# Kernel tuning notes

Measured on AMD Instinct MI355X. Metric: run time of the kernel, lower is better.

Reference implementation:

```python
import jax, jax.numpy as jnp
import numpy as np

N_EMBD = 2048
HEAD_DIM = 128
N_CTX = 2048
BATCH = 8
SEQ = 2048


def setup_inputs() -> dict:
    key = jax.random.key(0)
    ks = jax.random.split(key, 7)
    s = 1.0 / np.sqrt(N_EMBD)
    x = jax.random.normal(ks[0], (BATCH, SEQ, N_EMBD), dtype=jnp.float32)
    # torch Linear params: weight (out, in), bias (out,)
    Wq = jax.random.uniform(ks[1], (HEAD_DIM, N_EMBD), jnp.float32, -s, s)
    bq = jax.random.uniform(ks[2], (HEAD_DIM,), jnp.float32, -s, s)
    Wk = jax.random.uniform(ks[3], (HEAD_DIM, N_EMBD), jnp.float32, -s, s)
    bk = jax.random.uniform(ks[4], (HEAD_DIM,), jnp.float32, -s, s)
    Wv = jax.random.uniform(ks[5], (HEAD_DIM, N_EMBD), jnp.float32, -s, s)
    bv = jax.random.uniform(ks[6], (HEAD_DIM,), jnp.float32, -s, s)
    return {"x": x, "Wq": Wq, "bq": bq, "Wk": Wk, "bk": bk, "Wv": Wv, "bv": bv}


def reference(x, Wq, bq, Wk, bk, Wv, bv):
    # projections: y = x @ W^T + b
    q = jnp.einsum('bse,de->bsd', x, Wq) + bq  # (B, S, D)
    k = jnp.einsum('bse,de->bsd', x, Wk) + bk
    v = jnp.einsum('bse,de->bsd', x, Wv) + bv
    seq = x.shape[1]
    scores = jnp.einsum('bqd,bkd->bqk', q, k)  # (B, S, S)
    # causal mask: strictly-upper-triangular positions set to -inf (before scaling, as in source)
    causal = jnp.triu(jnp.ones((seq, seq), dtype=bool), k=1)
    scores = jnp.where(causal[None, :, :], -jnp.inf, scores)
    # NOTE: source scales by sqrt(seq_size), not sqrt(head_dim)
    weight = jax.nn.softmax(scores / jnp.sqrt(jnp.float32(seq)), axis=-1)
    return jnp.einsum('bqk,bkd->bqd', weight, v)
```

## Files before the change

kernel.cpp:

```cpp
#include <hip/hip_runtime.h>
#include <cmath>

#define BATCH 8
#define SEQ   2048
#define NEMB  2048
#define HD    128
#define NROWS (BATCH * SEQ)

typedef __bf16 v8bf __attribute__((ext_vector_type(8)));
typedef float  f32x4 __attribute__((ext_vector_type(4)));

union U8 { v8bf v; __bf16 b[8]; unsigned short e[8]; };
union F4 { f32x4 v; float f[4]; };

__device__ inline void async16(void* lds, const void* g) {
  __builtin_amdgcn_global_load_lds(
      (const __attribute__((address_space(1))) unsigned int*)g,
      (__attribute__((address_space(3))) unsigned int*)lds, 16, 0, 0);
}

__device__ inline v8bf cvt8(float4 a, float4 b) {
  U8 u;
  u.b[0] = (__bf16)a.x; u.b[1] = (__bf16)a.y; u.b[2] = (__bf16)a.z; u.b[3] = (__bf16)a.w;
  u.b[4] = (__bf16)b.x; u.b[5] = (__bf16)b.y; u.b[6] = (__bf16)b.z; u.b[7] = (__bf16)b.w;
  return u.v;
}

__global__ __launch_bounds__(256) void wconv_kernel(
    const float* __restrict__ Wq, const float* __restrict__ Wk,
    const float* __restrict__ Wv, __bf16* __restrict__ out) {
  const int id = blockIdx.x;
  const int proj = id >> 6, blk = id & 63;
  const float* __restrict__ W = proj == 0 ? Wq : proj == 1 ? Wk : Wv;
  __bf16* __restrict__ o = out + (size_t)proj * (HD * NEMB);
  const int base = blk * 4096 + threadIdx.x * 16;
  const float4* s = (const float4*)(W + base);
  float4 f0 = s[0], f1 = s[1], f2 = s[2], f3 = s[3];
  *(v8bf*)(o + base) = cvt8(f0, f1);
  *(v8bf*)(o + base + 8) = cvt8(f2, f3);
}

__global__ __launch_bounds__(512) void qkv_fused_kernel(
    const float* __restrict__ x, const __bf16* __restrict__ Wb,
    const float* __restrict__ bq, const float* __restrict__ bk,
    const float* __restrict__ bv,
    __bf16* __restrict__ Qb, __bf16* __restrict__ Kb, __bf16* __restrict__ Vb)
{
  const int bid0 = blockIdx.x;
  const int mt = ((bid0 & 7) << 5) + (bid0 >> 3);
  const int m0 = mt * 64;

  __shared__ char smem[131072];
  char* const A0 = smem;
  char* const A1 = smem + 16384;
  char* const Bu0 = smem + 32768;
  char* const Bu1 = smem + 81920;

  const int t = threadIdx.x, lane = t & 63, w = t >> 6;
  const int wm = w >> 2, wn4 = w & 3;
  const int hi = lane >> 4, lo = lane & 15;

  const float* pa[2];
  int laOff[2];
#pragma unroll
  for (int i = 0; i < 2; ++i) {
    const int j = w * 2 + i;
    const int r = j * 4 + (lane >> 4);
    const int c = (lane & 15) ^ (r & 7);
    pa[i] = x + (size_t)(m0 + r) * NEMB + c * 4;
    laOff[i] = j * 1024;
  }
  const __bf16* pb[6];
  int lbOff[6];
#pragma unroll
  for (int i = 0; i < 6; ++i) {
    const int j = w * 6 + i;
    const int r = j * 8 + (lane >> 3);
    const int pj = r >> 7, wr = r & 127;
    const int c = (lane & 7) ^ (r & 7);
    pb[i] = Wb + (size_t)pj * (HD * NEMB) + (size_t)wr * NEMB + c * 8;
    lbOff[i] = j * 1024;
  }

  f32x4 acc[2][6];
  const f32x4 fz = {0.f, 0.f, 0.f, 0.f};
#pragma unroll
  for (int m = 0; m < 2; ++m)
#pragma unroll
    for (int n = 0; n < 6; ++n) acc[m][n] = fz;

  auto STAGE = [&](int tt, char* Ab, char* Bb) {
    const int k0 = tt * 64;
#pragma unroll
    for (int i = 0; i < 2; ++i) async16(Ab + laOff[i], pa[i] + k0);
#pragma unroll
    for (int i = 0; i < 6; ++i) async16(Bb + lbOff[i], pb[i] + k0);
  };
  auto COMPUTE = [&](const char* Ab, const char* Bb) {
#pragma unroll
    for (int kk = 0; kk < 2; ++kk) {
      v8bf a[2], b[6];
#pragma unroll
      for (int m = 0; m < 2; ++m) {
        const int r = wm * 32 + m * 16 + lo;
        const int s = kk * 8 + hi * 2;
        const char* rowp = Ab + r * 256;
        F4 a0, a1;
        a0.v = *(const f32x4*)(rowp + (((s)     ^ (r & 7)) << 4));
        a1.v = *(const f32x4*)(rowp + (((s + 1) ^ (r & 7)) << 4));
        U8 u;
#pragma unroll
        for (int q = 0; q < 4; ++q) {
          u.b[q]     = (__bf16)a0.f[q];
          u.b[q + 4] = (__bf16)a1.f[q];
        }
        a[m] = u.v;
      }
      const int kc = kk * 4 + hi;
#pragma unroll
      for (int n = 0; n < 6; ++n) {
        const int r = wn4 * 96 + n * 16 + lo;
        b[n] = *(const v8bf*)(Bb + r * 128 + ((kc ^ (r & 7)) << 4));
      }
#pragma unroll
      for (int m = 0; m < 2; ++m)
#pragma unroll
        for (int n = 0; n < 6; ++n)
          acc[m][n] = __builtin_amdgcn_mfma_f32_16x16x32_bf16(a[m], b[n], acc[m][n], 0, 0, 0);
    }
  };

  const int NT = NEMB / 64;
  STAGE(0, A0, Bu0);
  for (int tt = 0; tt < NT; tt += 2) {
    __builtin_amdgcn_s_barrier();
    STAGE(tt + 1, A1, Bu1);
    asm volatile("s_waitcnt vmcnt(8)" ::: "memory");
    __builtin_amdgcn_s_barrier();
    COMPUTE(A0, Bu0);
    __builtin_amdgcn_s_barrier();
    if (tt + 2 < NT) {
      STAGE(tt + 2, A0, Bu0);
      asm volatile("s_waitcnt vmcnt(8)" ::: "memory");
    } else {
      asm volatile("s_waitcnt vmcnt(0)" ::: "memory");
    }
    __builtin_amdgcn_s_barrier();
    COMPUTE(A1, Bu1);
  }

#pragma unroll
  for (int n = 0; n < 6; ++n) {
    const int rrb = wn4 * 96 + n * 16;
    const int pj = rrb >> 7;
    const int col = (rrb & 127) + lo;
    __bf16* __restrict__ Out = pj == 0 ? Qb : pj == 1 ? Kb : Vb;
    const float* __restrict__ bias = pj == 0 ? bq : pj == 1 ? bk : bv;
    const float bi = bias[col];
#pragma unroll
    for (int m = 0; m < 2; ++m) {
#pragma unroll
      for (int r = 0; r < 4; ++r) {
        const int row = m0 + wm * 32 + m * 16 + hi * 4 + r;
        Out[(size_t)row * HD + col] = (__bf16)(acc[m][n][r] + bi);
      }
    }
  }
}

__global__ __launch_bounds__(256) void attn_kernel(
    const __bf16* __restrict__ Qb, const __bf16* __restrict__ Kb,
    const __bf16* __restrict__ Vb, __bf16* __restrict__ Opart,
    float* __restrict__ Ml)
{
  const int bid0 = blockIdx.x;
  const int bid = ((bid0 & 7) << 7) + (bid0 >> 3);
  const int b = bid >> 7;
  const int q = bid & 127;
  const int qt = q >> 2;
  const int s  = q & 3;
  const int q0 = qt * 64;
  const int kv_beg = (s * (qt + 1)) >> 2;
  const int kv_end = ((s + 1) * (qt + 1)) >> 2;
  const int nst = kv_end - kv_beg;

  const int t = threadIdx.x, lane = t & 63, w = t >> 6;
  const int hi = lane >> 4, lo = lane & 15;

  __shared__ __bf16 Ksm[2][64 * 128];
  __shared__ __bf16 Vtsm[2][128 * 64];
  __shared__ __bf16 Psm[4][16 * 64];

  v8bf aQ[4];
  {
    const __bf16* qp = Qb + ((size_t)(b * SEQ + q0 + w * 16 + lo)) * HD + hi * 8;
#pragma unroll
    for (int kk = 0; kk < 4; ++kk) aQ[kk] = *(const v8bf*)(qp + kk * 32);
  }

  const __bf16* kga[4];
#pragma unroll
  for (int i = 0; i < 4; ++i) {
    const int r = (w * 4 + i) * 4 + (lane >> 4);
    const int c = (lane & 15) ^ (r & 7);
    kga[i] = Kb + ((size_t)(b * SEQ) + r) * HD + c * 8;
  }

  const int keyg = t >> 4, dg = t & 15;
  U8 vv[4];

  f32x4 accO[8];
  const f32x4 fz = {0.f, 0.f, 0.f, 0.f};
#pragma unroll
  for (int n = 0; n < 8; ++n) accO[n] = fz;
  float m_s[4], l_s[4];
#pragma unroll
  for (int r = 0; r < 4; ++r) { m_s[r] = -INFINITY; l_s[r] = 0.f; }

  const float scale = 0.022097086912079608f;

  if (nst > 0) {
    auto STAGE_K = [&](int kv, int buf) {
      const size_t off = (size_t)kv * 64 * HD;
      char* kb = (char*)&Ksm[buf][0];
#pragma unroll
      for (int i = 0; i < 4; ++i) async16(kb + (w * 4 + i) * 1024, kga[i] + off);
    };
    auto LOAD_V = [&](int kv) {
      const __bf16* vp = Vb + ((size_t)(b * SEQ + kv * 64 + keyg * 4)) * HD + dg * 8;
#pragma unroll
      for (int j = 0; j < 4; ++j) vv[j].v = *(const v8bf*)(vp + (size_t)j * HD);
    };
    auto WRITE_VT = [&](int buf) {
      char* vb2 = (char*)&Vtsm[buf][0];
#pragma unroll
      for (int dd = 0; dd < 8; ++dd) {
        const int d = (dd + dg) & 7;
        ushort4 pk = make_ushort4(vv[0].e[d], vv[1].e[d], vv[2].e[d], vv[3].e[d]);
        const int row = dg * 8 + d;
        *(ushort4*)(vb2 + row * 128 + ((keyg * 8) ^ ((row & 7) << 4))) = pk;
      }
    };

    STAGE_K(kv_beg, 0);
    LOAD_V(kv_beg);
    WRITE_VT(0);
    __syncthreads();

    for (int t2 = 0; t2 < nst; ++t2) {
      const int kv = kv_beg + t2;
      const int cur = t2 & 1;
      const bool more = (t2 + 1 < nst);
      if (more) { STAGE_K(kv + 1, cur ^ 1); LOAD_V(kv + 1); }

      f32x4 accS[4];
#pragma unroll
      for (int n = 0; n < 4; ++n) accS[n] = fz;
      const char* ksm = (const char*)&Ksm[cur][0];
#pragma unroll
      for (int kk = 0; kk < 4; ++kk) {
        const int cb = kk * 64 + hi * 16;
        v8bf bk[4];
#pragma unroll
        for (int n = 0; n < 4; ++n) {
          const int r = n * 16 + lo;
          bk[n] = *(const v8bf*)(ksm + r * 256 + (cb ^ ((r & 7) << 4)));
        }
#pragma unroll
        for (int n = 0; n < 4; ++n)
          accS[n] = __builtin_amdgcn_mfma_f32_16x16x32_bf16(aQ[kk], bk[n], accS[n], 0, 0, 0);
      }

      float sv[4][4];
      const bool diag = (kv == qt);
#pragma unroll
      for (int n = 0; n < 4; ++n)
#pragma unroll
        for (int r = 0; r < 4; ++r) {
          float v = accS[n][r] * scale;
          if (diag) {
            const int key = kv * 64 + n * 16 + lo;
            const int qr = q0 + w * 16 + hi * 4 + r;
            if (key > qr) v = -INFINITY;
          }
          sv[n][r] = v;
        }

      float mx[4];
#pragma unroll
      for (int r = 0; r < 4; ++r) {
        mx[r] = fmaxf(fmaxf(sv[0][r], sv[1][r]), fmaxf(sv[2][r], sv[3][r]));
#pragma unroll
        for (int off = 1; off < 16; off <<= 1)
          mx[r] = fmaxf(mx[r], __shfl_xor(mx[r], off));
      }
      float corr[4], p[4][4], rs[4];
#pragma unroll
      for (int r = 0; r < 4; ++r) {
        const float mnew = fmaxf(m_s[r], mx[r]);
        corr[r] = __expf(m_s[r] - mnew);
        m_s[r] = mnew;
        rs[r] = 0.f;
      }
#pragma unroll
      for (int n = 0; n < 4; ++n)
#pragma unroll
        for (int r = 0; r < 4; ++r) {
          p[n][r] = __expf(sv[n][r] - m_s[r]);
          rs[r] += p[n][r];
        }
#pragma unroll
      for (int r = 0; r < 4; ++r) {
#pragma unroll
        for (int off = 1; off < 16; off <<= 1) rs[r] += __shfl_xor(rs[r], off);
        l_s[r] = l_s[r] * corr[r] + rs[r];
      }
#pragma unroll
      for (int n = 0; n < 8; ++n)
#pragma unroll
        for (int r = 0; r < 4; ++r) accO[n][r] *= corr[r];

#pragma unroll
      for (int n = 0; n < 4; ++n)
#pragma unroll
        for (int r = 0; r < 4; ++r) {
          const int row = hi * 4 + r;
          __bf16 h = (__bf16)p[n][r];
          *(unsigned short*)((char*)&Psm[w][0] + row * 128 +
                             (((n * 16 + lo) * 2) ^ ((row & 7) << 4))) =
              __builtin_bit_cast(unsigned short, h);
        }

      if (more) WRITE_VT(cur ^ 1);

      const char* vsm = (const char*)&Vtsm[cur][0];
#pragma unroll
      for (int k2 = 0; k2 < 2; ++k2) {
        const int cb = k2 * 64 + hi * 16;
        const v8bf aP = *(const v8bf*)((const char*)&Psm[w][0] + lo * 128 + (cb ^ ((lo & 7) << 4)));
#pragma unroll
        for (int n = 0; n < 8; ++n) {
          const int r = n * 16 + lo;
          const v8bf bv = *(const v8bf*)(vsm + r * 128 + (cb ^ ((r & 7) << 4)));
          accO[n] = __builtin_amdgcn_mfma_f32_16x16x32_bf16(aP, bv, accO[n], 0, 0, 0);
        }
      }
      if (more) __syncthreads();
    }
  }

#pragma unroll
  for (int r = 0; r < 4; ++r) {
    const int qr = q0 + w * 16 + hi * 4 + r;
    __bf16* op = Opart + ((size_t)s * NROWS + b * SEQ + qr) * HD + lo;
#pragma unroll
    for (int n = 0; n < 8; ++n) op[n * 16] = (__bf16)accO[n][r];
    if (lo == 0) {
      float* mlp = Ml + ((size_t)s * NROWS + b * SEQ + qr) * 2;
      mlp[0] = m_s[r];
      mlp[1] = l_s[r];
    }
  }
}

__global__ __launch_bounds__(256) void combine_kernel(
    const __bf16* __restrict__ Opart, const float* __restrict__ Ml,
    float* __restrict__ out)
{
  const int idx = blockIdx.x * 256 + threadIdx.x;
  const int row = idx >> 2, ch = idx & 3;
  float m[4], l[4];
#pragma unroll
  for (int s = 0; s < 4; ++s) {
    const float* mlp = Ml + ((size_t)s * NROWS + row) * 2;
    m[s] = mlp[0];
    l[s] = mlp[1];
  }
  const float M = fmaxf(fmaxf(m[0], m[1]), fmaxf(m[2], m[3]));
  float e[4], denom = 0.f;
#pragma unroll
  for (int s = 0; s < 4; ++s) { e[s] = __expf(m[s] - M); denom += l[s] * e[s]; }
  const float inv = 1.f / denom;

  float* po = out + (size_t)row * HD + ch * 32;
#pragma unroll
  for (int j = 0; j < 4; ++j) {
    float sum[8];
#pragma unroll
    for (int q2 = 0; q2 < 8; ++q2) sum[q2] = 0.f;
#pragma unroll
    for (int s = 0; s < 4; ++s) {
      U8 o;
      o.v = *(const v8bf*)(Opart + ((size_t)s * NROWS + row) * HD + ch * 32 + j * 8);
#pragma unroll
      for (int q2 = 0; q2 < 8; ++q2) sum[q2] += (float)o.b[q2] * e[s];
    }
#pragma unroll
    for (int q2 = 0; q2 < 8; ++q2) po[j * 8 + q2] = sum[q2] * inv;
  }
}

extern "C" void kernel_launch(void* const* d_in, const int* in_sizes, int n_in,
                              void* d_out, int out_size, void* d_ws, size_t ws_size,
                              hipStream_t stream) {
  const float* x  = (const float*)d_in[0];
  const float* Wq = (const float*)d_in[1];
  const float* bq = (const float*)d_in[2];
  const float* Wk = (const float*)d_in[3];
  const float* bk = (const float*)d_in[4];
  const float* Wv = (const float*)d_in[5];
  const float* bv = (const float*)d_in[6];
  float* out = (float*)d_out;

  __bf16* Qb = (__bf16*)d_ws;
  __bf16* Kb = Qb + (size_t)NROWS * HD;
  __bf16* Vb = Kb + (size_t)NROWS * HD;
  __bf16* Wb = Vb + (size_t)NROWS * HD;
  __bf16* Opart = Wb + (size_t)3 * HD * NEMB;
  float*  Ml = (float*)(Opart + (size_t)4 * NROWS * HD);

  wconv_kernel<<<dim3(3 * 64), dim3(256), 0, stream>>>(Wq, Wk, Wv, Wb);
  qkv_fused_kernel<<<dim3(256), dim3(512), 0, stream>>>(
      x, Wb, bq, bk, bv, Qb, Kb, Vb);
  attn_kernel<<<dim3(BATCH * 32 * 4), dim3(256), 0, stream>>>(Qb, Kb, Vb, Opart, Ml);
  combine_kernel<<<dim3(NROWS * 4 / 256), dim3(256), 0, stream>>>(Opart, Ml, out);
}
```

Baseline: 111.3 us.

## Prepack weights in MFMA fragment order and load B directly into registers

The weight conversion kernel now writes bf16 weights in the exact per-lane MFMA fragment layout, so the QKV projection kernel loads B operands straight from global memory into registers with coalesced 16-byte loads instead of staging them through LDS. LDS use drops from 128 KB to 32 KB, holding only the fp32 activation tiles, which removes the B-side LDS reads and writes and may allow higher occupancy. In exchange each wave keeps 24 extra vector registers of double-buffered B fragments, and B-fragment reuse now comes from L2 across waves rather than from shared LDS.

```diff
diff --git a/kernel.cpp b/kernel.cpp
--- a/kernel.cpp
+++ b/kernel.cpp
@@ -26,22 +26,26 @@
   return u.v;
 }
 
-__global__ __launch_bounds__(256) void wconv_kernel(
+__global__ __launch_bounds__(256) void wpack_kernel(
     const float* __restrict__ Wq, const float* __restrict__ Wk,
-    const float* __restrict__ Wv, __bf16* __restrict__ out) {
-  const int id = blockIdx.x;
-  const int proj = id >> 6, blk = id & 63;
-  const float* __restrict__ W = proj == 0 ? Wq : proj == 1 ? Wk : Wv;
-  __bf16* __restrict__ o = out + (size_t)proj * (HD * NEMB);
-  const int base = blk * 4096 + threadIdx.x * 16;
-  const float4* s = (const float4*)(W + base);
-  float4 f0 = s[0], f1 = s[1], f2 = s[2], f3 = s[3];
-  *(v8bf*)(o + base) = cvt8(f0, f1);
-  *(v8bf*)(o + base + 8) = cvt8(f2, f3);
+    const float* __restrict__ Wv, __bf16* __restrict__ wp) {
+  const int g = blockIdx.x * 256 + threadIdx.x;
+  const int lane = g & 63;
+  const int u = g >> 6;
+  const int kk = u & 1;
+  const int tt = (u >> 1) & 31;
+  const int nf = (u >> 6) & 7;
+  const int p  = u >> 9;
+  const float* __restrict__ W = p == 0 ? Wq : p == 1 ? Wk : Wv;
+  const int row = nf * 16 + (lane & 15);
+  const int k   = tt * 64 + kk * 32 + (lane >> 4) * 8;
+  const float4* s = (const float4*)(W + (size_t)row * NEMB + k);
+  float4 f0 = s[0], f1 = s[1];
+  *(v8bf*)(wp + (size_t)g * 8) = cvt8(f0, f1);
 }
 
 __global__ __launch_bounds__(512) void qkv_fused_kernel(
-    const float* __restrict__ x, const __bf16* __restrict__ Wb,
+    const float* __restrict__ x, const __bf16* __restrict__ Wp,
     const float* __restrict__ bq, const float* __restrict__ bk,
     const float* __restrict__ bv,
     __bf16* __restrict__ Qb, __bf16* __restrict__ Kb, __bf16* __restrict__ Vb)
@@ -50,11 +54,7 @@
   const int mt = ((bid0 & 7) << 5) + (bid0 >> 3);
   const int m0 = mt * 64;
 
-  __shared__ char smem[131072];
-  char* const A0 = smem;
-  char* const A1 = smem + 16384;
-  char* const Bu0 = smem + 32768;
-  char* const Bu1 = smem + 81920;
+  __shared__ float Asm[2][64 * 64];
 
   const int t = threadIdx.x, lane = t & 63, w = t >> 6;
   const int wm = w >> 2, wn4 = w & 3;
@@ -70,17 +70,8 @@
     pa[i] = x + (size_t)(m0 + r) * NEMB + c * 4;
     laOff[i] = j * 1024;
   }
-  const __bf16* pb[6];
-  int lbOff[6];
-#pragma unroll
-  for (int i = 0; i < 6; ++i) {
-    const int j = w * 6 + i;
-    const int r = j * 8 + (lane >> 3);
-    const int pj = r >> 7, wr = r & 127;
-    const int c = (lane & 7) ^ (r & 7);
-    pb[i] = Wb + (size_t)pj * (HD * NEMB) + (size_t)wr * NEMB + c * 8;
-    lbOff[i] = j * 1024;
-  }
+
+  const __bf16* bb = Wp + lane * 8;
 
   f32x4 acc[2][6];
   const f32x4 fz = {0.f, 0.f, 0.f, 0.f};
@@ -89,17 +80,25 @@
 #pragma unroll
     for (int n = 0; n < 6; ++n) acc[m][n] = fz;
 
-  auto STAGE = [&](int tt, char* Ab, char* Bb) {
+  v8bf B0[6][2], B1[6][2];
+  auto LOADB = [&](v8bf (&B)[6][2], int tt) {
+#pragma unroll
+    for (int n = 0; n < 6; ++n)
+#pragma unroll
+      for (int kk = 0; kk < 2; ++kk)
+        B[n][kk] = *(const v8bf*)(bb + (size_t)((wn4 * 6 + n) * 64 + tt * 2 + kk) * 512);
+  };
+  auto STAGE_A = [&](int tt, int buf) {
     const int k0 = tt * 64;
-#pragma unroll
-    for (int i = 0; i < 2; ++i) async16(Ab + laOff[i], pa[i] + k0);
-#pragma unroll
-    for (int i = 0; i < 6; ++i) async16(Bb + lbOff[i], pb[i] + k0);
+    char* base = (char*)&Asm[buf][0];
+#pragma unroll
+    for (int i = 0; i < 2; ++i) async16(base + laOff[i], pa[i] + k0);
   };
-  auto COMPUTE = [&](const char* Ab, const char* Bb) {
+  auto COMPUTE = [&](int buf, v8bf (&B)[6][2]) {
+    const char* Ab = (const char*)&Asm[buf][0];
 #pragma unroll
     for (int kk = 0; kk < 2; ++kk) {
-      v8bf a[2], b[6];
+      v8bf a[2];
 #pragma unroll
       for (int m = 0; m < 2; ++m) {
         const int r = wm * 32 + m * 16 + lo;
@@ -116,37 +115,34 @@
         }
         a[m] = u.v;
       }
-      const int kc = kk * 4 + hi;
-#pragma unroll
-      for (int n = 0; n < 6; ++n) {
-        const int r = wn4 * 96 + n * 16 + lo;
-        b[n] = *(const v8bf*)(Bb + r * 128 + ((kc ^ (r & 7)) << 4));
-      }
 #pragma unroll
       for (int m = 0; m < 2; ++m)
 #pragma unroll
         for (int n = 0; n < 6; ++n)
-          acc[m][n] = __builtin_amdgcn_mfma_f32_16x16x32_bf16(a[m], b[n], acc[m][n], 0, 0, 0);
+          acc[m][n] = __builtin_amdgcn_mfma_f32_16x16x32_bf16(a[m], B[n][kk], acc[m][n], 0, 0, 0);
     }
   };
 
   const int NT = NEMB / 64;
-  STAGE(0, A0, Bu0);
+  STAGE_A(0, 0);
+  LOADB(B0, 0);
   for (int tt = 0; tt < NT; tt += 2) {
     __builtin_amdgcn_s_barrier();
-    STAGE(tt + 1, A1, Bu1);
-    asm volatile("s_waitcnt vmcnt(8)" ::: "memory");
+    STAGE_A(tt + 1, 1);
+    LOADB(B1, tt + 1);
+    asm volatile("s_waitcnt vmcnt(14)" ::: "memory");
     __builtin_amdgcn_s_barrier();
-    COMPUTE(A0, Bu0);
+    COMPUTE(0, B0);
     __builtin_amdgcn_s_barrier();
     if (tt + 2 < NT) {
-      STAGE(tt + 2, A0, Bu0);
-      asm volatile("s_waitcnt vmcnt(8)" ::: "memory");
+      STAGE_A(tt + 2, 0);
+      LOADB(B0, tt + 2);
+      asm volatile("s_waitcnt vmcnt(14)" ::: "memory");
     } else {
       asm volatile("s_waitcnt vmcnt(0)" ::: "memory");
     }
     __builtin_amdgcn_s_barrier();
-    COMPUTE(A1, Bu1);
+    COMPUTE(1, B1);
   }
 
 #pragma unroll
@@ -415,13 +411,13 @@
   __bf16* Qb = (__bf16*)d_ws;
   __bf16* Kb = Qb + (size_t)NROWS * HD;
   __bf16* Vb = Kb + (size_t)NROWS * HD;
-  __bf16* Wb = Vb + (size_t)NROWS * HD;
-  __bf16* Opart = Wb + (size_t)3 * HD * NEMB;
+  __bf16* Wp = Vb + (size_t)NROWS * HD;
+  __bf16* Opart = Wp + (size_t)1536 * 512;
   float*  Ml = (float*)(Opart + (size_t)4 * NROWS * HD);
 
-  wconv_kernel<<<dim3(3 * 64), dim3(256), 0, stream>>>(Wq, Wk, Wv, Wb);
+  wpack_kernel<<<dim3(384), dim3(256), 0, stream>>>(Wq, Wk, Wv, Wp);
   qkv_fused_kernel<<<dim3(256), dim3(512), 0, stream>>>(
-      x, Wb, bq, bk, bv, Qb, Kb, Vb);
+      x, Wp, bq, bk, bv, Qb, Kb, Vb);
   attn_kernel<<<dim3(BATCH * 32 * 4), dim3(256), 0, stream>>>(Qb, Kb, Vb, Opart, Ml);
   combine_kernel<<<dim3(NROWS * 4 / 256), dim3(256), 0, stream>>>(Opart, Ml, out);
 }
```

New measurement: 124.1 us. 11.5% more time.
